# Kernel tuning notes

Hardware: AMD Instinct MI355X
Metric: run time of the kernel (lower is better)

The kernel has to match this reference:

```python
import jax, jax.numpy as jnp
import numpy as np
import math

B, S, H = 4, 2048, 1024
NH, HD = 16, 64
BASE = 10000.0

def _rope_cos_sin(seq_len, dim):
    inv_freq = 1.0 / (BASE ** (jnp.arange(0, dim, 2, dtype=jnp.float32) / dim))
    pos = jnp.arange(seq_len, dtype=jnp.float32)
    freqs = jnp.outer(pos, inv_freq)              # [S, dim/2]
    emb = jnp.concatenate([freqs, freqs], axis=-1)  # [S, dim]
    return jnp.cos(emb), jnp.sin(emb)

def _apply_rotary(x, cos, sin):
    # x: [B, NH, S, HD]; cos/sin: [S, HD]
    d = x.shape[-1] // 2
    x1, x2 = x[..., :d], x[..., d:]
    rotated = jnp.concatenate([-x2, x1], axis=-1)
    return x * cos[None, None] + rotated * sin[None, None]

def setup_inputs() -> dict:
    key = jax.random.key(0)
    ks = jax.random.split(key, 5)
    scale = 1.0 / math.sqrt(H)
    return {
        "x": jax.random.normal(ks[0], (B, S, H), dtype=jnp.float32),
        "attention_mask": jnp.ones((B, S), dtype=jnp.int32),
        "Wq": jax.random.normal(ks[1], (H, H), dtype=jnp.float32) * scale,
        "Wk": jax.random.normal(ks[2], (H, H), dtype=jnp.float32) * scale,
        "Wv": jax.random.normal(ks[3], (H, H), dtype=jnp.float32) * scale,
        "Wo": jax.random.normal(ks[4], (H, H), dtype=jnp.float32) * scale,
    }

def reference(x, attention_mask, Wq, Wk, Wv, Wo):
    b, s, _ = x.shape
    # projections (nn.Linear: x @ W.T)
    q = (x @ Wq.T).reshape(b, s, NH, HD).transpose(0, 2, 1, 3)  # [B,NH,S,HD]
    k = (x @ Wk.T).reshape(b, s, NH, HD).transpose(0, 2, 1, 3)
    v = (x @ Wv.T).reshape(b, s, NH, HD).transpose(0, 2, 1, 3)
    cos, sin = _rope_cos_sin(s, HD)
    q = _apply_rotary(q, cos, sin)
    k = _apply_rotary(k, cos, sin)
    scores = jnp.einsum('bhqd,bhkd->bhqk', q, k) / math.sqrt(HD)
    mask = attention_mask[:, None, None, :]  # [B,1,1,S]
    scores = jnp.where(mask == 0, -jnp.inf, scores)
    attn = jax.nn.softmax(scores, axis=-1)
    out = jnp.einsum('bhqk,bhkd->bhqd', attn, v)
    out = out.transpose(0, 2, 1, 3).reshape(b, s, NH * HD)
    return out @ Wo.T
```

## Files before the change

### kernel.cpp

```cpp
#include <hip/hip_runtime.h>
#include <hip/hip_bf16.h>

#define B_  4
#define S_  2048
#define H_  1024
#define NH_ 16
#define HD_ 64

typedef __bf16 bf16;
typedef __attribute__((ext_vector_type(8))) __bf16 bf16x8;
typedef __attribute__((ext_vector_type(4))) __bf16 bf16x4;
typedef __attribute__((ext_vector_type(4))) float f32x4;

typedef const __attribute__((address_space(1))) char* gptr_t;
typedef __attribute__((address_space(3))) char* lptr_t;
#define GLOAD_LDS16(g, l) __builtin_amdgcn_global_load_lds((gptr_t)(g), (lptr_t)(l), 16, 0, 0)

__device__ __forceinline__ f32x4 mfma16(bf16x8 a, bf16x8 b, f32x4 c) {
    return __builtin_amdgcn_mfma_f32_16x16x32_bf16(a, b, c, 0, 0, 0);
}

__global__ void k_cvt(const float* __restrict__ src, bf16* __restrict__ dst, int n4) {
    int i = blockIdx.x * blockDim.x + threadIdx.x;
    if (i < n4) {
        float4 v = ((const float4*)src)[i];
        bf16x4 o;
        o[0] = (__bf16)v.x; o[1] = (__bf16)v.y; o[2] = (__bf16)v.z; o[3] = (__bf16)v.w;
        *(bf16x4*)(dst + i * 4) = o;
    }
}

__global__ void k_tab(float* __restrict__ cosT, float* __restrict__ sinT) {
    int i = blockIdx.x * blockDim.x + threadIdx.x;
    if (i >= S_ * 32) return;
    int s = i >> 5, d = i & 31;
    float inv = powf(10000.0f, -(float)d * (1.0f / 32.0f));
    float ang = (float)s * inv;
    cosT[i] = cosf(ang);
    sinT[i] = sinf(ang);
}

template<int EPI>
__global__ __launch_bounds__(256) void k_gemm(
        const bf16* __restrict__ A, const bf16* __restrict__ Bw,
        bf16* __restrict__ q_out, bf16* __restrict__ k_out, bf16* __restrict__ v_out,
        const float* __restrict__ cosT, const float* __restrict__ sinT,
        float* __restrict__ fout) {
    __shared__ bf16 As[128 * 32];
    __shared__ bf16 Bs[128 * 32];
    const int t = threadIdx.x, l = t & 63, w = t >> 6;
    const int lr = l & 15, hi = l >> 4;
    const int m0 = blockIdx.y * 128, n0 = blockIdx.x * 128;
    const int wr = (w >> 1) * 64, wc = (w & 1) * 64;
    f32x4 acc[4][4] = {};

    for (int k0 = 0; k0 < 1024; k0 += 32) {
        __syncthreads();
#pragma unroll
        for (int i = 0; i < 2; ++i) {
            int o = i * 4096 + t * 16;
            int row = o >> 6, colb = o & 63;
            GLOAD_LDS16((const char*)A + ((size_t)(m0 + row) * 1024 + k0) * 2 + colb,
                        (char*)As + o);
            GLOAD_LDS16((const char*)Bw + ((size_t)(n0 + row) * 1024 + k0) * 2 + colb,
                        (char*)Bs + o);
        }
        __syncthreads();
        bf16x8 af[4], bfr[4];
#pragma unroll
        for (int mi = 0; mi < 4; ++mi)
            af[mi] = *(const bf16x8*)&As[(wr + mi * 16 + lr) * 32 + hi * 8];
#pragma unroll
        for (int ni = 0; ni < 4; ++ni)
            bfr[ni] = *(const bf16x8*)&Bs[(wc + ni * 16 + lr) * 32 + hi * 8];
#pragma unroll
        for (int mi = 0; mi < 4; ++mi)
#pragma unroll
            for (int ni = 0; ni < 4; ++ni)
                acc[mi][ni] = mfma16(af[mi], bfr[ni], acc[mi][ni]);
    }

    if (EPI == 0) {
        const int nbase = n0 + wc;
        const int which = nbase >> 10;
        const int head = (nbase & 1023) >> 6;
        if (which == 2) {
#pragma unroll
            for (int mi = 0; mi < 4; ++mi) {
                int m = m0 + wr + mi * 16 + hi * 4;
                int bb = m >> 11, s = m & 2047;
                size_t vbase = (size_t)(bb * NH_ + head) * HD_;
#pragma unroll
                for (int ni = 0; ni < 4; ++ni) {
                    bf16x4 o;
#pragma unroll
                    for (int r = 0; r < 4; ++r) o[r] = (__bf16)acc[mi][ni][r];
                    *(bf16x4*)(v_out + (vbase + ni * 16 + lr) * (size_t)S_ + s) = o;
                }
            }
        } else {
            bf16* dst = which == 0 ? q_out : k_out;
#pragma unroll
            for (int mi = 0; mi < 4; ++mi) {
#pragma unroll
                for (int r = 0; r < 4; ++r) {
                    int m = m0 + wr + mi * 16 + hi * 4 + r;
                    int bb = m >> 11, s = m & 2047;
                    size_t base = (((size_t)bb * NH_ + head) * S_ + s) * HD_;
#pragma unroll
                    for (int ni = 0; ni < 2; ++ni) {
                        int d = ni * 16 + lr;
                        float c = cosT[s * 32 + d], sn = sinT[s * 32 + d];
                        float x1 = acc[mi][ni][r], x2 = acc[mi][ni + 2][r];
                        dst[base + d]      = (__bf16)(x1 * c - x2 * sn);
                        dst[base + d + 32] = (__bf16)(x2 * c + x1 * sn);
                    }
                }
            }
        }
    } else {
#pragma unroll
        for (int mi = 0; mi < 4; ++mi)
#pragma unroll
            for (int ni = 0; ni < 4; ++ni)
#pragma unroll
                for (int r = 0; r < 4; ++r)
                    fout[(size_t)(m0 + wr + mi * 16 + hi * 4 + r) * 1024
                         + (n0 + wc + ni * 16 + lr)] = acc[mi][ni][r];
    }
}

__global__ __launch_bounds__(256, 3) void k_attn(
        const bf16* __restrict__ qr, const bf16* __restrict__ kr,
        const bf16* __restrict__ vt, const int* __restrict__ mask,
        bf16* __restrict__ aout) {
    __shared__ bf16 Ks[2][64 * 64];
    __shared__ bf16 Vs[2][64 * 64];
    const int t = threadIdx.x, l = t & 63, w = t >> 6;
    const int lr = l & 15, hi = l >> 4;
    const int sw = (lr & 7) << 4;
    const int bh = blockIdx.y, b = bh >> 4, head = bh & 15;
    const int qbase = blockIdx.x * 128 + w * 32;

    const bf16* Qb = qr + (size_t)bh * S_ * HD_;
    const char* Kg = (const char*)(kr + (size_t)bh * S_ * HD_);
    const char* Vg = (const char*)(vt + (size_t)bh * HD_ * S_);
    const int* mrow = mask + b * S_;

    bf16x8 qf[2][2];
#pragma unroll
    for (int qh = 0; qh < 2; ++qh)
#pragma unroll
        for (int h = 0; h < 2; ++h) {
            qf[qh][h] = *(const bf16x8*)(Qb + (size_t)(qbase + qh * 16 + lr) * HD_ + h * 32 + hi * 8);
#pragma unroll
            for (int j = 0; j < 8; ++j)
                qf[qh][h][j] = (__bf16)((float)qf[qh][h][j] * 0.125f);
        }

    int anyz0 = 0;
    for (int i = l; i < S_; i += 64) anyz0 |= (mrow[i] == 0);
    const bool anyz = __any(anyz0);

    f32x4 acc[4][2] = {};
    float mrun[2] = {-1e30f, -1e30f};
    float lrun[2] = {0.0f, 0.0f};

    auto STAGE = [&](int buf, int kv0) {
#pragma unroll
        for (int i = 0; i < 2; ++i) {
            int o = i * 4096 + t * 16;
            int row = o >> 7, colb = o & 127;
            int scol = colb ^ ((row & 7) << 4);
            GLOAD_LDS16(Kg + (size_t)(kv0 + row) * 128 + scol, (char*)Ks[buf] + o);
            GLOAD_LDS16(Vg + (size_t)row * (S_ * 2) + (size_t)kv0 * 2 + scol,
                        (char*)Vs[buf] + o);
        }
    };

    STAGE(0, 0);
    const int NT = S_ / 64;
    for (int ti = 0; ti < NT; ++ti) {
        __syncthreads();
        if (ti + 1 < NT) STAGE((ti + 1) & 1, (ti + 1) * 64);
        const char* Kc = (const char*)Ks[ti & 1];
        const char* Vc = (const char*)Vs[ti & 1];
        const int kv0 = ti * 64;

        f32x4 st[4][2] = {};
#pragma unroll
        for (int g = 0; g < 4; ++g) {
            int rb = (g * 16 + lr) * 128;
            bf16x8 kf0 = *(const bf16x8*)(Kc + rb + ((hi * 16) ^ sw));
            bf16x8 kf1 = *(const bf16x8*)(Kc + rb + ((64 + hi * 16) ^ sw));
            st[g][0] = mfma16(kf0, qf[0][0], st[g][0]);
            st[g][0] = mfma16(kf1, qf[0][1], st[g][0]);
            st[g][1] = mfma16(kf0, qf[1][0], st[g][1]);
            st[g][1] = mfma16(kf1, qf[1][1], st[g][1]);
        }

        if (anyz) {
#pragma unroll
            for (int g = 0; g < 4; ++g) {
                int4 mv = *(const int4*)(mrow + kv0 + g * 16 + hi * 4);
#pragma unroll
                for (int qh = 0; qh < 2; ++qh) {
                    st[g][qh][0] = mv.x ? st[g][qh][0] : -INFINITY;
                    st[g][qh][1] = mv.y ? st[g][qh][1] : -INFINITY;
                    st[g][qh][2] = mv.z ? st[g][qh][2] : -INFINITY;
                    st[g][qh][3] = mv.w ? st[g][qh][3] : -INFINITY;
                }
            }
        }

        float tm[2];
#pragma unroll
        for (int qh = 0; qh < 2; ++qh) {
            float m_ = st[0][qh][0];
#pragma unroll
            for (int g = 0; g < 4; ++g)
#pragma unroll
                for (int r = 0; r < 4; ++r) m_ = fmaxf(m_, st[g][qh][r]);
            m_ = fmaxf(m_, __shfl_xor(m_, 16));
            m_ = fmaxf(m_, __shfl_xor(m_, 32));
            tm[qh] = m_;
        }

        bool need = (tm[0] > mrun[0] + 8.0f) || (tm[1] > mrun[1] + 8.0f);
        if (__any(need)) {
#pragma unroll
            for (int qh = 0; qh < 2; ++qh) {
                float mn = fmaxf(mrun[qh], tm[qh]);
                float corr = __expf(mrun[qh] - mn);
                lrun[qh] *= corr;
#pragma unroll
                for (int dt = 0; dt < 4; ++dt) acc[dt][qh] *= corr;
                mrun[qh] = mn;
            }
        }

        bf16x8 pB[2][2];
#pragma unroll
        for (int qh = 0; qh < 2; ++qh) {
            float ts = 0.0f;
#pragma unroll
            for (int g = 0; g < 4; ++g)
#pragma unroll
                for (int r = 0; r < 4; ++r) {
                    float e = __expf(st[g][qh][r] - mrun[qh]);
                    pB[qh][g >> 1][(g & 1) * 4 + r] = (__bf16)e;
                    ts += e;
                }
            ts += __shfl_xor(ts, 16);
            ts += __shfl_xor(ts, 32);
            lrun[qh] += ts;
        }

#pragma unroll
        for (int dt = 0; dt < 4; ++dt) {
            const char* vrow = Vc + (dt * 16 + lr) * 128;
#pragma unroll
            for (int ks = 0; ks < 2; ++ks) {
                bf16x4 va = *(const bf16x4*)(vrow + ((ks * 64 + hi * 8) ^ sw));
                bf16x4 vb = *(const bf16x4*)(vrow + ((ks * 64 + 32 + hi * 8) ^ sw));
                bf16x8 vf;
#pragma unroll
                for (int j = 0; j < 4; ++j) { vf[j] = va[j]; vf[4 + j] = vb[j]; }
                acc[dt][0] = mfma16(vf, pB[0][ks], acc[dt][0]);
                acc[dt][1] = mfma16(vf, pB[1][ks], acc[dt][1]);
            }
        }
    }

    float inv[2] = {1.0f / lrun[0], 1.0f / lrun[1]};
#pragma unroll
    for (int qh = 0; qh < 2; ++qh) {
        size_t obase = ((size_t)(b * S_ + qbase + qh * 16 + lr)) * H_ + head * HD_;
#pragma unroll
        for (int dt = 0; dt < 4; ++dt) {
            bf16x4 o;
#pragma unroll
            for (int r = 0; r < 4; ++r) o[r] = (__bf16)(acc[dt][qh][r] * inv[qh]);
            *(bf16x4*)(aout + obase + dt * 16 + hi * 4) = o;
        }
    }
}

extern "C" void kernel_launch(void* const* d_in, const int* in_sizes, int n_in,
                              void* d_out, int out_size, void* d_ws, size_t ws_size,
                              hipStream_t stream) {
    const float* x  = (const float*)d_in[0];
    const int* mask = (const int*)d_in[1];
    const float* Wq = (const float*)d_in[2];
    const float* Wk = (const float*)d_in[3];
    const float* Wv = (const float*)d_in[4];
    const float* Wo = (const float*)d_in[5];
    float* out = (float*)d_out;

    char* ws = (char*)d_ws;
    bf16* xb    = (bf16*)ws;
    bf16* wqkv  = (bf16*)(ws + (size_t)16 * 1048576);
    bf16* wob   = (bf16*)(ws + (size_t)22 * 1048576);
    bf16* qr    = (bf16*)(ws + (size_t)24 * 1048576);
    bf16* kr    = (bf16*)(ws + (size_t)40 * 1048576);
    bf16* vtw   = (bf16*)(ws + (size_t)56 * 1048576);
    float* cosT = (float*)(ws + (size_t)72 * 1048576);
    float* sinT = (float*)(ws + (size_t)72 * 1048576 + 262144);

    k_cvt<<<2097152 / 256, 256, 0, stream>>>(x, xb, 2097152);
    k_cvt<<<262144 / 256, 256, 0, stream>>>(Wq, wqkv, 262144);
    k_cvt<<<262144 / 256, 256, 0, stream>>>(Wk, wqkv + 1048576, 262144);
    k_cvt<<<262144 / 256, 256, 0, stream>>>(Wv, wqkv + 2097152, 262144);
    k_cvt<<<262144 / 256, 256, 0, stream>>>(Wo, wob, 262144);
    k_tab<<<256, 256, 0, stream>>>(cosT, sinT);

    k_gemm<0><<<dim3(24, 64), 256, 0, stream>>>(xb, wqkv, qr, kr, vtw, cosT, sinT, nullptr);

    k_attn<<<dim3(16, 64), 256, 0, stream>>>(qr, kr, vtw, mask, xb);

    k_gemm<1><<<dim3(8, 64), 256, 0, stream>>>(xb, wob, nullptr, nullptr, nullptr,
                                               nullptr, nullptr, out);
}
```

Before: 245.1 us.

## Permute V layout for 16-byte LDS reads, fold Q scale into RoPE, swizzle block IDs

V is now stored with sequence positions permuted inside each 64-wide block. The attention kernel can then fetch each V fragment with a single 16-byte LDS read instead of two 8-byte reads plus a merge. The 1/sqrt(d) query scaling moves into the QKV GEMM RoPE epilogue, which removes the per-block bf16 rescale of Q. Both kernels remap block IDs in a strided XCD-aware order to improve L2 locality, and the mask scan reads int4 vectors. The V permutation must match the P fragment ordering exactly, otherwise results are wrong.

```diff
diff --git a/kernel.cpp b/kernel.cpp
--- a/kernel.cpp
+++ b/kernel.cpp
@@ -18,6 +18,15 @@
 
 __device__ __forceinline__ f32x4 mfma16(bf16x8 a, bf16x8 b, f32x4 c) {
     return __builtin_amdgcn_mfma_f32_16x16x32_bf16(a, b, c, 0, 0, 0);
+}
+
+__device__ __forceinline__ void swz_bid(int& bx, int& by) {
+    const int gx = gridDim.x;
+    const int nwg = gx * gridDim.y;
+    const int i = blockIdx.x + gx * blockIdx.y;
+    const int w = (i & 7) * (nwg >> 3) + (i >> 3);
+    bx = w % gx;
+    by = w / gx;
 }
 
 __global__ void k_cvt(const float* __restrict__ src, bf16* __restrict__ dst, int n4) {
@@ -50,7 +59,9 @@
     __shared__ bf16 Bs[128 * 32];
     const int t = threadIdx.x, l = t & 63, w = t >> 6;
     const int lr = l & 15, hi = l >> 4;
-    const int m0 = blockIdx.y * 128, n0 = blockIdx.x * 128;
+    int bx, by;
+    swz_bid(bx, by);
+    const int m0 = by * 128, n0 = bx * 128;
     const int wr = (w >> 1) * 64, wc = (w & 1) * 64;
     f32x4 acc[4][4] = {};
 
@@ -89,17 +100,21 @@
             for (int mi = 0; mi < 4; ++mi) {
                 int m = m0 + wr + mi * 16 + hi * 4;
                 int bb = m >> 11, s = m & 2047;
+                int st = s & 63;
+                int pos = ((st >> 5) & 1) * 32 + ((st >> 2) & 3) * 8 + ((st >> 4) & 1) * 4;
+                int sp = (s & ~63) | pos;
                 size_t vbase = (size_t)(bb * NH_ + head) * HD_;
 #pragma unroll
                 for (int ni = 0; ni < 4; ++ni) {
                     bf16x4 o;
 #pragma unroll
                     for (int r = 0; r < 4; ++r) o[r] = (__bf16)acc[mi][ni][r];
-                    *(bf16x4*)(v_out + (vbase + ni * 16 + lr) * (size_t)S_ + s) = o;
+                    *(bf16x4*)(v_out + (vbase + ni * 16 + lr) * (size_t)S_ + sp) = o;
                 }
             }
         } else {
             bf16* dst = which == 0 ? q_out : k_out;
+            const float qsc = which == 0 ? 0.125f : 1.0f;
 #pragma unroll
             for (int mi = 0; mi < 4; ++mi) {
 #pragma unroll
@@ -110,7 +125,7 @@
 #pragma unroll
                     for (int ni = 0; ni < 2; ++ni) {
                         int d = ni * 16 + lr;
-                        float c = cosT[s * 32 + d], sn = sinT[s * 32 + d];
+                        float c = cosT[s * 32 + d] * qsc, sn = sinT[s * 32 + d] * qsc;
                         float x1 = acc[mi][ni][r], x2 = acc[mi][ni + 2][r];
                         dst[base + d]      = (__bf16)(x1 * c - x2 * sn);
                         dst[base + d + 32] = (__bf16)(x2 * c + x1 * sn);
@@ -139,8 +154,10 @@
     const int t = threadIdx.x, l = t & 63, w = t >> 6;
     const int lr = l & 15, hi = l >> 4;
     const int sw = (lr & 7) << 4;
-    const int bh = blockIdx.y, b = bh >> 4, head = bh & 15;
-    const int qbase = blockIdx.x * 128 + w * 32;
+    int bx, by;
+    swz_bid(bx, by);
+    const int bh = by, b = bh >> 4, head = bh & 15;
+    const int qbase = bx * 128 + w * 32;
 
     const bf16* Qb = qr + (size_t)bh * S_ * HD_;
     const char* Kg = (const char*)(kr + (size_t)bh * S_ * HD_);
@@ -151,15 +168,14 @@
 #pragma unroll
     for (int qh = 0; qh < 2; ++qh)
 #pragma unroll
-        for (int h = 0; h < 2; ++h) {
+        for (int h = 0; h < 2; ++h)
             qf[qh][h] = *(const bf16x8*)(Qb + (size_t)(qbase + qh * 16 + lr) * HD_ + h * 32 + hi * 8);
-#pragma unroll
-            for (int j = 0; j < 8; ++j)
-                qf[qh][h][j] = (__bf16)((float)qf[qh][h][j] * 0.125f);
-        }
 
     int anyz0 = 0;
-    for (int i = l; i < S_; i += 64) anyz0 |= (mrow[i] == 0);
+    for (int i = l; i < S_ / 4; i += 64) {
+        int4 m4 = ((const int4*)mrow)[i];
+        anyz0 |= (m4.x == 0) | (m4.y == 0) | (m4.z == 0) | (m4.w == 0);
+    }
     const bool anyz = __any(anyz0);
 
     f32x4 acc[4][2] = {};
@@ -261,11 +277,7 @@
             const char* vrow = Vc + (dt * 16 + lr) * 128;
 #pragma unroll
             for (int ks = 0; ks < 2; ++ks) {
-                bf16x4 va = *(const bf16x4*)(vrow + ((ks * 64 + hi * 8) ^ sw));
-                bf16x4 vb = *(const bf16x4*)(vrow + ((ks * 64 + 32 + hi * 8) ^ sw));
-                bf16x8 vf;
-#pragma unroll
-                for (int j = 0; j < 4; ++j) { vf[j] = va[j]; vf[4 + j] = vb[j]; }
+                bf16x8 vf = *(const bf16x8*)(vrow + ((ks * 64 + hi * 16) ^ sw));
                 acc[dt][0] = mfma16(vf, pB[0][ks], acc[dt][0]);
                 acc[dt][1] = mfma16(vf, pB[1][ks], acc[dt][1]);
             }
```

Measured after the change: 235.8 us. 1.04x faster.
